# Kernel tuning notes

Hardware: AMD Instinct MI355X
Metric: run time of the kernel (lower is better)

The kernel has to match this reference:

```python
import jax, jax.numpy as jnp
import numpy as np

VOCAB, D_MODEL, DICT, TOP_K = 50257, 512, 16384, 32
N_CONCEPTS, N_RELATIONS = 16, 6
B, S = 1024, 32


def sparse_topk(coeffs, top_k):
    # abs-topk along last dim, keep signed values, scatter to dense
    _, idx = jax.lax.top_k(jnp.abs(coeffs), top_k)          # [B, k]
    signed = jnp.take_along_axis(coeffs, idx, axis=-1)      # [B, k]
    rows = jnp.arange(coeffs.shape[0])[:, None]
    return jnp.zeros_like(coeffs).at[rows, idx].set(signed)


def setup_inputs() -> dict:
    key = jax.random.key(0)
    ks = jax.random.split(key, 16)
    f = lambda k, shape, scale: jax.random.normal(k, shape, dtype=jnp.float32) * scale
    inp = {
        'clean_tokens': jax.random.randint(ks[0], (B, S), 0, VOCAB),
        'noisy_tokens': jax.random.randint(ks[1], (B, S), 0, VOCAB),
        'embedding': f(ks[2], (VOCAB, D_MODEL), 1.0),
        'enc_w1': f(ks[3], (D_MODEL, D_MODEL), D_MODEL ** -0.5),
        'enc_b1': jnp.zeros((D_MODEL,), jnp.float32),
        'enc_w2': f(ks[4], (D_MODEL, D_MODEL), D_MODEL ** -0.5),
        'enc_b2': jnp.zeros((D_MODEL,), jnp.float32),
        'shared_atoms': f(ks[5], (DICT, D_MODEL), 0.04),
        'router_w': f(ks[6], (DICT, D_MODEL), D_MODEL ** -0.5),
        'concept_delta_w': f(ks[7], (DICT, D_MODEL), D_MODEL ** -0.5),
        'relation_delta_w': f(ks[8], (DICT, D_MODEL), D_MODEL ** -0.5),
        'concept_head_w': f(ks[9], (N_CONCEPTS, D_MODEL), D_MODEL ** -0.5),
        'concept_head_b': jnp.zeros((N_CONCEPTS,), jnp.float32),
        'relation_head_w': f(ks[10], (N_RELATIONS, D_MODEL), D_MODEL ** -0.5),
        'relation_head_b': jnp.zeros((N_RELATIONS,), jnp.float32),
    }
    return inp


def reference(clean_tokens, noisy_tokens, embedding, enc_w1, enc_b1, enc_w2, enc_b2,
              shared_atoms, router_w, concept_delta_w, relation_delta_w,
              concept_head_w, concept_head_b, relation_head_w, relation_head_b):
    def pooled(tokens):
        x = embedding[tokens].mean(axis=1)                       # [B, D]
        h = jax.nn.silu(x @ enc_w1.T + enc_b1)
        return h @ enc_w2.T + enc_b2

    def encode(p, delta_w):
        coeffs = p @ router_w.T + 0.3 * (p @ delta_w.T)          # [B, DICT]
        sparse = sparse_topk(coeffs, TOP_K)
        rep = sparse @ shared_atoms                              # [B, D]
        return rep, sparse

    clean_p = pooled(clean_tokens)
    noisy_p = pooled(noisy_tokens)
    c_rep, c_sp = encode(clean_p, concept_delta_w)
    r_rep, r_sp = encode(clean_p, relation_delta_w)
    nc_rep, nc_sp = encode(noisy_p, concept_delta_w)
    nr_rep, nr_sp = encode(noisy_p, relation_delta_w)

    fused_clean = 0.2 * clean_p + 0.9 * c_rep + 0.9 * r_rep
    fused_noisy = 0.2 * noisy_p + 0.9 * nc_rep + 0.9 * nr_rep

    return (fused_clean @ concept_head_w.T + concept_head_b,
            fused_clean @ relation_head_w.T + relation_head_b,
            fused_noisy @ concept_head_w.T + concept_head_b,
            fused_noisy @ relation_head_w.T + relation_head_b,
            c_sp, r_sp, nc_sp, nr_sp)
```

## Files before the change

### kernel.cpp

```cpp
#include <hip/hip_runtime.h>


typedef _Float16 f16x8 __attribute__((ext_vector_type(8)));
typedef _Float16 f16x4 __attribute__((ext_vector_type(4)));
typedef float f32x4 __attribute__((ext_vector_type(4)));

#define OUT_SPARSE 45056
#define SPARSE_PER 16777216

#define ASYNC16(gp, lp) __builtin_amdgcn_global_load_lds(                      \
    (const __attribute__((address_space(1))) void*)(gp),                       \
    (__attribute__((address_space(3))) void*)(lp), 16, 0, 0)

__device__ inline float h2f(unsigned s) {
    _Float16 h = __builtin_bit_cast(_Float16, (unsigned short)(s & 0xFFFFu));
    return (float)h;
}

__global__ __launch_bounds__(128) void pool_kernel(
    const int* __restrict__ ct, const int* __restrict__ nt,
    const float* __restrict__ emb, double* __restrict__ xout)
{
    const int row = blockIdx.x, s = blockIdx.y;
    const int tid = threadIdx.x;
    __shared__ int tk[32];
    const int* t = (s ? nt : ct) + row * 32;
    if (tid < 32) tk[tid] = t[tid];
    __syncthreads();
    const int d = tid * 4;
    double a0 = 0, a1 = 0, a2 = 0, a3 = 0;
    for (int i = 0; i < 32; ++i) {
        const float4 v = *(const float4*)(emb + (size_t)tk[i] * 512 + d);
        a0 += (double)v.x; a1 += (double)v.y; a2 += (double)v.z; a3 += (double)v.w;
    }
    double* o = xout + ((size_t)s * 1024 + row) * 512 + d;
    o[0] = a0 * 0.03125; o[1] = a1 * 0.03125; o[2] = a2 * 0.03125; o[3] = a3 * 0.03125;
}

__global__ __launch_bounds__(256) void enc_gemm(
    const double* __restrict__ A, const float* __restrict__ W,
    const float* __restrict__ bias, double* __restrict__ C,
    _Float16* __restrict__ C16, int act)
{
    __shared__ double Ask[16][68];
    __shared__ double Wsk[16][68];
    const int tid = threadIdx.x;
    const int m0 = blockIdx.y * 64, n0 = blockIdx.x * 64;
    const int ty = tid >> 4, tx = tid & 15;
    const int r = tid >> 2, c4 = (tid & 3) * 4;
    double acc[4][4] = {};
    for (int k0 = 0; k0 < 512; k0 += 16) {
        const double4 av = *(const double4*)(A + (size_t)(m0 + r) * 512 + k0 + c4);
        const float4  wv = *(const float4*) (W + (size_t)(n0 + r) * 512 + k0 + c4);
        __syncthreads();
        Ask[c4 + 0][r] = av.x; Ask[c4 + 1][r] = av.y; Ask[c4 + 2][r] = av.z; Ask[c4 + 3][r] = av.w;
        Wsk[c4 + 0][r] = (double)wv.x; Wsk[c4 + 1][r] = (double)wv.y;
        Wsk[c4 + 2][r] = (double)wv.z; Wsk[c4 + 3][r] = (double)wv.w;
        __syncthreads();
#pragma unroll
        for (int k = 0; k < 16; ++k) {
            const double4 a = *(const double4*)&Ask[k][ty * 4];
            const double4 b = *(const double4*)&Wsk[k][tx * 4];
            const double aa[4] = {a.x, a.y, a.z, a.w};
            const double bb[4] = {b.x, b.y, b.z, b.w};
#pragma unroll
            for (int i = 0; i < 4; ++i)
#pragma unroll
                for (int j = 0; j < 4; ++j) acc[i][j] += aa[i] * bb[j];
        }
    }
#pragma unroll
    for (int i = 0; i < 4; ++i) {
        const int row = m0 + ty * 4 + i;
#pragma unroll
        for (int j = 0; j < 4; ++j) {
            const int col = n0 + tx * 4 + j;
            double v = acc[i][j] + (double)bias[col];
            if (act) v = v / (1.0 + exp(-v));
            C[(size_t)row * 512 + col] = v;
            if (C16) C16[(size_t)row * 512 + col] = (_Float16)v;
        }
    }
}

__global__ __launch_bounds__(256) void combine_kernel(
    const float* __restrict__ router, const float* __restrict__ cd,
    const float* __restrict__ rd, _Float16* __restrict__ wc,
    _Float16* __restrict__ wr, float* __restrict__ wcf,
    float* __restrict__ wrf)
{
    const size_t i = ((size_t)blockIdx.x * 256 + threadIdx.x) * 4;
    if (i >= (size_t)16384 * 512) return;
    const float4 r = *(const float4*)(router + i);
    const float4 c = *(const float4*)(cd + i);
    const float4 d = *(const float4*)(rd + i);
    const float4 fc = { r.x + 0.3f * c.x, r.y + 0.3f * c.y, r.z + 0.3f * c.z, r.w + 0.3f * c.w };
    const float4 fr = { r.x + 0.3f * d.x, r.y + 0.3f * d.y, r.z + 0.3f * d.z, r.w + 0.3f * d.w };
    f16x4 hc = { (_Float16)fc.x, (_Float16)fc.y, (_Float16)fc.z, (_Float16)fc.w };
    f16x4 hr = { (_Float16)fr.x, (_Float16)fr.y, (_Float16)fr.z, (_Float16)fr.w };
    *(f16x4*)(wc + i) = hc;
    *(f16x4*)(wr + i) = hr;
    *(float4*)(wcf + i) = fc;
    *(float4*)(wrf + i) = fr;
}

__global__ __launch_bounds__(256) void approx_gemm(
    const _Float16* __restrict__ P, const _Float16* __restrict__ Wc,
    const _Float16* __restrict__ Wr, unsigned* __restrict__ candg)
{
    __shared__ _Float16 ABs[8192];
    __shared__ _Float16 Cst[128 * 128];
    __shared__ unsigned ecnt[128];
    _Float16* As = ABs;
    _Float16* Bs = ABs + 4096;

    const int tid = threadIdx.x;
    const int q = blockIdx.z;
    const int n0 = blockIdx.x * 128, m0 = blockIdx.y * 128;
    const _Float16* A = P + (size_t)(q >> 1) * 524288;
    const _Float16* B = (q & 1) ? Wr : Wc;

    const int lane = tid & 63, w = tid >> 6;
    const int wm = w & 1, wn = w >> 1;
    const int lr = lane & 15, lk = lane >> 4;

    const int ch0 = w * 2, ch1 = w * 2 + 1;
    const int lrow = lane >> 2, lh = (lane & 3) * 8;
    const _Float16* Ag0 = A + (size_t)(m0 + ch0 * 16 + lrow) * 512 + lh;
    const _Float16* Ag1 = A + (size_t)(m0 + ch1 * 16 + lrow) * 512 + lh;
    const _Float16* Bg0 = B + (size_t)(n0 + ch0 * 16 + lrow) * 512 + lh;
    const _Float16* Bg1 = B + (size_t)(n0 + ch1 * 16 + lrow) * 512 + lh;
    _Float16* Al0 = As + ch0 * 512;
    _Float16* Al1 = As + ch1 * 512;
    _Float16* Bl0 = Bs + ch0 * 512;
    _Float16* Bl1 = Bs + ch1 * 512;

    const f32x4 zero = {0.f, 0.f, 0.f, 0.f};
    f32x4 acc[4][4];
#pragma unroll
    for (int i = 0; i < 4; ++i)
#pragma unroll
        for (int j = 0; j < 4; ++j) acc[i][j] = zero;

    for (int kt = 0; kt < 16; ++kt) {
        const int k0 = kt * 32;
        __syncthreads();
        ASYNC16(Ag0 + k0, Al0);
        ASYNC16(Ag1 + k0, Al1);
        ASYNC16(Bg0 + k0, Bl0);
        ASYNC16(Bg1 + k0, Bl1);
        __syncthreads();
        f16x8 af[4], bf[4];
#pragma unroll
        for (int i = 0; i < 4; ++i) af[i] = *(const f16x8*)(As + (wm * 64 + i * 16 + lr) * 32 + lk * 8);
#pragma unroll
        for (int j = 0; j < 4; ++j) bf[j] = *(const f16x8*)(Bs + (wn * 64 + j * 16 + lr) * 32 + lk * 8);
#pragma unroll
        for (int i = 0; i < 4; ++i)
#pragma unroll
            for (int j = 0; j < 4; ++j)
                acc[i][j] = __builtin_amdgcn_mfma_f32_16x16x32_f16(af[i], bf[j], acc[i][j], 0, 0, 0);
    }
    __syncthreads();
#pragma unroll
    for (int i = 0; i < 4; ++i)
#pragma unroll
        for (int j = 0; j < 4; ++j)
#pragma unroll
            for (int rr = 0; rr < 4; ++rr)
                Cst[(wm * 64 + i * 16 + lk * 4 + rr) * 128 + (wn * 64 + j * 16 + lr)] =
                    (_Float16)acc[i][j][rr];
    if (tid < 128) ecnt[tid] = 0;
    __syncthreads();

    const int r = tid >> 1, h = tid & 1;
    const unsigned* cr = (const unsigned*)(Cst + r * 128 + h * 64);
    float ss = 0.f;
#pragma unroll
    for (int j = 0; j < 32; ++j) {
        const unsigned u = cr[j];
        const float f0 = h2f(u), f1 = h2f(u >> 16);
        ss = fmaf(f0, f0, fmaf(f1, f1, ss));
    }
    ss += __shfl_xor(ss, 1);
    const _Float16 hc = (_Float16)(2.0f * sqrtf(ss * (1.f / 128.f)));
    const unsigned cutk = (unsigned)__builtin_bit_cast(unsigned short, hc) & 0x7FFFu;
    unsigned* emit = (unsigned*)ABs;
    const int colbase = n0 + h * 64;
#pragma unroll
    for (int j = 0; j < 32; ++j) {
        const unsigned u = cr[j];
        const unsigned k0 = u & 0x7FFFu, k1 = (u >> 16) & 0x7FFFu;
        if (k0 >= cutk && k0) {
            const unsigned pos = atomicAdd(&ecnt[r], 1u);
            if (pos < 32u) emit[r * 32 + pos] = (k0 << 16) | (unsigned)(16383 - (colbase + 2 * j));
        }
        if (k1 >= cutk && k1) {
            const unsigned pos = atomicAdd(&ecnt[r], 1u);
            if (pos < 32u) emit[r * 32 + pos] = (k1 << 16) | (unsigned)(16383 - (colbase + 2 * j + 1));
        }
    }
    __syncthreads();
    {
        const unsigned c = min(ecnt[r], 32u);
#pragma unroll
        for (int s2 = 0; s2 < 16; ++s2) {
            const unsigned sl = (unsigned)(h * 16 + s2);
            if (sl >= c) emit[r * 32 + sl] = 0u;
        }
        unsigned* eg = candg + (((size_t)q * 1024 + m0 + r) * 128 + blockIdx.x) * 32;
        const uint4* e4 = (const uint4*)(emit + r * 32 + h * 16);
        uint4* g4 = (uint4*)(eg + h * 16);
        g4[0] = e4[0]; g4[1] = e4[1]; g4[2] = e4[2]; g4[3] = e4[3];
    }
}

__global__ __launch_bounds__(256) void select_kernel(
    const double* __restrict__ pw, const float* __restrict__ wcf,
    const float* __restrict__ wrf, const unsigned* __restrict__ candg,
    const float* __restrict__ atoms, float* __restrict__ selvw,
    int* __restrict__ seliw, float* __restrict__ repw)
{
    constexpr int NCAP = 160, NRE = 64;
    const int row = blockIdx.x, q = blockIdx.y;
    const int pset = q >> 1;
    const int tid = threadIdx.x;

    __shared__ unsigned hist[1024];
    __shared__ unsigned pscan[256];
    __shared__ double prow[512];
    __shared__ unsigned cent[NCAP];
    __shared__ int r64i[NRE];
    __shared__ double cval[NRE];
    __shared__ float selv[32];
    __shared__ int seli[32];
    __shared__ int cnt, bstar;

    const double* prg = pw + ((size_t)pset * 1024 + row) * 512;
    const unsigned* crow = candg + ((size_t)q * 1024 + row) * 4096;

    for (int b = tid; b < 1024; b += 256) hist[b] = 0;
    if (tid == 0) { cnt = 0; bstar = -1; }
    if (tid < NRE) r64i[tid] = 0;
    prow[tid] = prg[tid];
    prow[tid + 256] = prg[tid + 256];

    uint4 cv[4];
#pragma unroll
    for (int p = 0; p < 4; ++p) cv[p] = ((const uint4*)crow)[p * 256 + tid];
    __syncthreads();

#pragma unroll
    for (int p = 0; p < 4; ++p) {
        const unsigned ee[4] = {cv[p].x, cv[p].y, cv[p].z, cv[p].w};
#pragma unroll
        for (int e = 0; e < 4; ++e)
            if (ee[e]) atomicAdd(&hist[ee[e] >> 21], 1u);
    }
    __syncthreads();

    const unsigned h0 = hist[tid * 4], h1 = hist[tid * 4 + 1];
    const unsigned h2 = hist[tid * 4 + 2], h3 = hist[tid * 4 + 3];
    const unsigned l3 = h3, l2 = h2 + l3, l1 = h1 + l2, l0 = h0 + l1;
    pscan[tid] = l0;
    __syncthreads();
    for (int s = 1; s < 256; s <<= 1) {
        const unsigned v = (tid + s < 256) ? pscan[tid + s] : 0u;
        __syncthreads();
        pscan[tid] += v;
        __syncthreads();
    }
    {
        const unsigned above = (tid < 255) ? pscan[tid + 1] : 0u;
        int best = -1;
        if (l0 + above >= 64u) best = tid * 4;
        if (l1 + above >= 64u) best = tid * 4 + 1;
        if (l2 + above >= 64u) best = tid * 4 + 2;
        if (l3 + above >= 64u) best = tid * 4 + 3;
        if (best >= 0) atomicMax(&bstar, best);
    }
    __syncthreads();
    const unsigned kmin = (unsigned)(bstar < 0 ? 1 : bstar) << 5;

#pragma unroll
    for (int p = 0; p < 4; ++p) {
        const unsigned ee[4] = {cv[p].x, cv[p].y, cv[p].z, cv[p].w};
#pragma unroll
        for (int e = 0; e < 4; ++e) {
            if (ee[e] && (ee[e] >> 16) >= kmin) {
                const int pos = atomicAdd(&cnt, 1);
                if (pos < NCAP) cent[pos] = ee[e];
            }
        }
    }
    __syncthreads();
    const int nc = min(cnt, NCAP);

    for (int p = tid; p < nc; p += 256) {
        const unsigned e = cent[p];
        int rr = 0;
        for (int j = 0; j < nc; ++j) rr += (cent[j] > e) ? 1 : 0;
        if (rr < NRE) r64i[rr] = 16383 - (int)(e & 0xFFFFu);
    }
    __syncthreads();

    const float* wsel = (q & 1) ? wrf : wcf;
    const int w = tid >> 6, lane = tid & 63;
    for (int c = w; c < NRE; c += 4) {
        const int idx = r64i[c];
        const float4* rp4 = (const float4*)(wsel + (size_t)idx * 512);
        const float4 r0 = rp4[lane * 2], r1 = rp4[lane * 2 + 1];
        const double* pv = prow + lane * 8;
        double aR = pv[0] * (double)r0.x + pv[1] * (double)r0.y + pv[2] * (double)r0.z + pv[3] * (double)r0.w
                  + pv[4] * (double)r1.x + pv[5] * (double)r1.y + pv[6] * (double)r1.z + pv[7] * (double)r1.w;
        for (int sh = 32; sh > 0; sh >>= 1) aR += __shfl_down(aR, sh);
        if (lane == 0) cval[c] = aR;
    }
    __syncthreads();

    if (tid < NRE) {
        const double av = fabs(cval[tid]);
        const int mi = r64i[tid];
        int rr = 0;
        for (int j = 0; j < NRE; ++j) {
            const double aj = fabs(cval[j]);
            rr += (aj > av || (aj == av && r64i[j] < mi)) ? 1 : 0;
        }
        if (rr < 32) { selv[rr] = (float)cval[tid]; seli[rr] = mi; }
    }
    __syncthreads();
    if (tid < 32) {
        const size_t sb = ((size_t)q * 1024 + row) * 32 + tid;
        selvw[sb] = selv[tid];
        seliw[sb] = seli[tid];
    }

    double a0 = 0, a1 = 0;
    for (int k = 0; k < 32; ++k) {
        const double v = (double)selv[k];
        const float* ar = atoms + (size_t)seli[k] * 512;
        a0 += v * (double)ar[tid];
        a1 += v * (double)ar[tid + 256];
    }
    float* rp = repw + ((size_t)q * 1024 + row) * 512;
    rp[tid] = (float)a0;
    rp[tid + 256] = (float)a1;
}

__global__ __launch_bounds__(256) void zero_kernel(float4* __restrict__ p, unsigned n4)
{
    const float4 z = {0.f, 0.f, 0.f, 0.f};
    unsigned i = blockIdx.x * 256u + threadIdx.x;
    const unsigned stride = gridDim.x * 256u;
    for (; i < n4; i += stride) p[i] = z;
}

__global__ __launch_bounds__(256) void heads_kernel(
    const double* __restrict__ pw, const float* __restrict__ repw,
    const float* __restrict__ chw, const float* __restrict__ chb,
    const float* __restrict__ rhw, const float* __restrict__ rhb,
    const float* __restrict__ selvw, const int* __restrict__ seliw,
    float* __restrict__ out)
{
    const int row = blockIdx.x, s = blockIdx.y;
    const int tid = threadIdx.x;
    __shared__ double fused[512];

    if (tid < 64) {
        const int qq = s * 2 + (tid >> 5), k = tid & 31;
        const size_t sb = ((size_t)qq * 1024 + row) * 32 + k;
        out[(size_t)OUT_SPARSE + (size_t)qq * SPARSE_PER + (size_t)row * 16384 + (size_t)seliw[sb]] = selvw[sb];
    }

    const double* pr = pw + ((size_t)s * 1024 + row) * 512;
    const float* rc = repw + ((size_t)(s * 2 + 0) * 1024 + row) * 512;
    const float* rr = repw + ((size_t)(s * 2 + 1) * 1024 + row) * 512;
    for (int d = tid; d < 512; d += 256)
        fused[d] = 0.2 * pr[d] + 0.9 * (double)rc[d] + 0.9 * (double)rr[d];
    __syncthreads();
    const int w = tid >> 6, lane = tid & 63;
    for (int o = w; o < 22; o += 4) {
        const float* hw2 = (o < 16) ? (chw + (size_t)o * 512) : (rhw + (size_t)(o - 16) * 512);
        double acc = 0;
#pragma unroll
        for (int j = 0; j < 8; ++j) acc += fused[lane + 64 * j] * (double)hw2[lane + 64 * j];
        for (int sh = 32; sh > 0; sh >>= 1) acc += __shfl_down(acc, sh);
        if (lane == 0) {
            if (o < 16) out[(s ? 22528 : 0) + row * 16 + o] = (float)(acc + (double)chb[o]);
            else        out[(s ? 38912 : 16384) + row * 6 + (o - 16)] = (float)(acc + (double)rhb[o - 16]);
        }
    }
}

extern "C" void kernel_launch(void* const* d_in, const int* in_sizes, int n_in,
                              void* d_out, int out_size, void* d_ws, size_t ws_size,
                              hipStream_t stream)
{
    const int*   ctok   = (const int*)d_in[0];
    const int*   ntok   = (const int*)d_in[1];
    const float* emb    = (const float*)d_in[2];
    const float* w1     = (const float*)d_in[3];
    const float* b1     = (const float*)d_in[4];
    const float* w2     = (const float*)d_in[5];
    const float* b2     = (const float*)d_in[6];
    const float* atoms  = (const float*)d_in[7];
    const float* router = (const float*)d_in[8];
    const float* cdelta = (const float*)d_in[9];
    const float* rdelta = (const float*)d_in[10];
    const float* chw    = (const float*)d_in[11];
    const float* chb    = (const float*)d_in[12];
    const float* rhw    = (const float*)d_in[13];
    const float* rhb    = (const float*)d_in[14];
    float* out = (float*)d_out;

    float*    wcf   = out + OUT_SPARSE;
    float*    wrf   = wcf + 8388608;
    unsigned* candg = (unsigned*)(wrf + 8388608);

    double*    xw   = (double*)d_ws;
    double*    hw   = xw + 1048576;
    double*    pw   = hw + 1048576;
    float*     repw = (float*)(pw + 1048576);
    _Float16*  pf16 = (_Float16*)(repw + 2097152);
    _Float16*  wcw  = pf16 + 1048576;
    _Float16*  wrw  = wcw + 8388608;
    float*     selvw = (float*)hw;
    int*       seliw = (int*)(selvw + 131072);

    pool_kernel<<<dim3(1024, 2), 128, 0, stream>>>(ctok, ntok, emb, xw);
    enc_gemm<<<dim3(8, 32), 256, 0, stream>>>(xw, w1, b1, hw, (_Float16*)nullptr, 1);
    enc_gemm<<<dim3(8, 32), 256, 0, stream>>>(hw, w2, b2, pw, pf16, 0);
    combine_kernel<<<8192, 256, 0, stream>>>(router, cdelta, rdelta, wcw, wrw, wcf, wrf);
    approx_gemm<<<dim3(128, 8, 4), 256, 0, stream>>>(pf16, wcw, wrw, candg);
    select_kernel<<<dim3(1024, 4), 256, 0, stream>>>(pw, wcf, wrf, candg, atoms, selvw, seliw, repw);
    zero_kernel<<<2048, 256, 0, stream>>>((float4*)(out + OUT_SPARSE), (unsigned)SPARSE_PER);
    heads_kernel<<<dim3(1024, 2), 256, 0, stream>>>(pw, repw, chw, chb, rhw, rhb, selvw, seliw, out);
}
```

Before: 876.7 us.

## Swizzle 64-wide K tiles, filter candidates in registers, fuse sparse zeroing into heads

Measured after the change: 873.0 us. About the same (-0.4%).

```diff
diff --git a/kernel.cpp b/kernel.cpp
--- a/kernel.cpp
+++ b/kernel.cpp
@@ -11,11 +11,6 @@
 #define ASYNC16(gp, lp) __builtin_amdgcn_global_load_lds(                      \
     (const __attribute__((address_space(1))) void*)(gp),                       \
     (__attribute__((address_space(3))) void*)(lp), 16, 0, 0)
-
-__device__ inline float h2f(unsigned s) {
-    _Float16 h = __builtin_bit_cast(_Float16, (unsigned short)(s & 0xFFFFu));
-    return (float)h;
-}
 
 __global__ __launch_bounds__(128) void pool_kernel(
     const int* __restrict__ ct, const int* __restrict__ nt,
@@ -108,32 +103,38 @@
     const _Float16* __restrict__ P, const _Float16* __restrict__ Wc,
     const _Float16* __restrict__ Wr, unsigned* __restrict__ candg)
 {
-    __shared__ _Float16 ABs[8192];
-    __shared__ _Float16 Cst[128 * 128];
+    __shared__ _Float16 As[8192];
+    __shared__ _Float16 Bs[8192];
+    __shared__ float    ssp[128][2];
+    __shared__ unsigned cutk_s[128];
     __shared__ unsigned ecnt[128];
-    _Float16* As = ABs;
-    _Float16* Bs = ABs + 4096;
 
     const int tid = threadIdx.x;
     const int q = blockIdx.z;
     const int n0 = blockIdx.x * 128, m0 = blockIdx.y * 128;
-    const _Float16* A = P + (size_t)(q >> 1) * 524288;
-    const _Float16* B = (q & 1) ? Wr : Wc;
+    const _Float16* Agbl = P + (size_t)(q >> 1) * 524288;
+    const _Float16* Bgbl = (q & 1) ? Wr : Wc;
 
     const int lane = tid & 63, w = tid >> 6;
     const int wm = w & 1, wn = w >> 1;
     const int lr = lane & 15, lk = lane >> 4;
-
-    const int ch0 = w * 2, ch1 = w * 2 + 1;
-    const int lrow = lane >> 2, lh = (lane & 3) * 8;
-    const _Float16* Ag0 = A + (size_t)(m0 + ch0 * 16 + lrow) * 512 + lh;
-    const _Float16* Ag1 = A + (size_t)(m0 + ch1 * 16 + lrow) * 512 + lh;
-    const _Float16* Bg0 = B + (size_t)(n0 + ch0 * 16 + lrow) * 512 + lh;
-    const _Float16* Bg1 = B + (size_t)(n0 + ch1 * 16 + lrow) * 512 + lh;
-    _Float16* Al0 = As + ch0 * 512;
-    _Float16* Al1 = As + ch1 * 512;
-    _Float16* Bl0 = Bs + ch0 * 512;
-    _Float16* Bl1 = Bs + ch1 * 512;
+    const int xr = lr & 7;
+
+    const int srow = lane >> 3;
+    const int cg = (lane & 7) ^ srow;
+    const _Float16* ag[4];
+    const _Float16* bg[4];
+    _Float16* al[4];
+    _Float16* bl[4];
+#pragma unroll
+    for (int i = 0; i < 4; ++i) {
+        const int G = i * 4 + w;
+        const int rr0 = G * 8 + srow;
+        ag[i] = Agbl + (size_t)(m0 + rr0) * 512 + cg * 8;
+        bg[i] = Bgbl + (size_t)(n0 + rr0) * 512 + cg * 8;
+        al[i] = As + G * 512;
+        bl[i] = Bs + G * 512;
+    }
 
     const f32x4 zero = {0.f, 0.f, 0.f, 0.f};
     f32x4 acc[4][4];
@@ -142,75 +143,82 @@
 #pragma unroll
         for (int j = 0; j < 4; ++j) acc[i][j] = zero;
 
-    for (int kt = 0; kt < 16; ++kt) {
-        const int k0 = kt * 32;
-        __syncthreads();
-        ASYNC16(Ag0 + k0, Al0);
-        ASYNC16(Ag1 + k0, Al1);
-        ASYNC16(Bg0 + k0, Bl0);
-        ASYNC16(Bg1 + k0, Bl1);
-        __syncthreads();
-        f16x8 af[4], bf[4];
-#pragma unroll
-        for (int i = 0; i < 4; ++i) af[i] = *(const f16x8*)(As + (wm * 64 + i * 16 + lr) * 32 + lk * 8);
-#pragma unroll
-        for (int j = 0; j < 4; ++j) bf[j] = *(const f16x8*)(Bs + (wn * 64 + j * 16 + lr) * 32 + lk * 8);
-#pragma unroll
-        for (int i = 0; i < 4; ++i)
+    for (int kt = 0; kt < 8; ++kt) {
+        const int k0 = kt * 64;
+        __syncthreads();
+#pragma unroll
+        for (int i = 0; i < 4; ++i) ASYNC16(ag[i] + k0, al[i]);
+#pragma unroll
+        for (int i = 0; i < 4; ++i) ASYNC16(bg[i] + k0, bl[i]);
+        __syncthreads();
+#pragma unroll
+        for (int kk = 0; kk < 2; ++kk) {
+            f16x8 af[4], bf[4];
+#pragma unroll
+            for (int i = 0; i < 4; ++i)
+                af[i] = *(const f16x8*)(As + (wm * 64 + i * 16 + lr) * 64 + (((kk << 2) | lk) ^ xr) * 8);
 #pragma unroll
             for (int j = 0; j < 4; ++j)
-                acc[i][j] = __builtin_amdgcn_mfma_f32_16x16x32_f16(af[i], bf[j], acc[i][j], 0, 0, 0);
-    }
-    __syncthreads();
+                bf[j] = *(const f16x8*)(Bs + (wn * 64 + j * 16 + lr) * 64 + (((kk << 2) | lk) ^ xr) * 8);
+#pragma unroll
+            for (int i = 0; i < 4; ++i)
+#pragma unroll
+                for (int j = 0; j < 4; ++j)
+                    acc[i][j] = __builtin_amdgcn_mfma_f32_16x16x32_f16(af[i], bf[j], acc[i][j], 0, 0, 0);
+        }
+    }
+
+    if (tid < 128) ecnt[tid] = 0;
 #pragma unroll
     for (int i = 0; i < 4; ++i)
 #pragma unroll
-        for (int j = 0; j < 4; ++j)
-#pragma unroll
-            for (int rr = 0; rr < 4; ++rr)
-                Cst[(wm * 64 + i * 16 + lk * 4 + rr) * 128 + (wn * 64 + j * 16 + lr)] =
-                    (_Float16)acc[i][j][rr];
-    if (tid < 128) ecnt[tid] = 0;
-    __syncthreads();
-
-    const int r = tid >> 1, h = tid & 1;
-    const unsigned* cr = (const unsigned*)(Cst + r * 128 + h * 64);
-    float ss = 0.f;
-#pragma unroll
-    for (int j = 0; j < 32; ++j) {
-        const unsigned u = cr[j];
-        const float f0 = h2f(u), f1 = h2f(u >> 16);
-        ss = fmaf(f0, f0, fmaf(f1, f1, ss));
-    }
-    ss += __shfl_xor(ss, 1);
-    const _Float16 hc = (_Float16)(2.0f * sqrtf(ss * (1.f / 128.f)));
-    const unsigned cutk = (unsigned)__builtin_bit_cast(unsigned short, hc) & 0x7FFFu;
-    unsigned* emit = (unsigned*)ABs;
-    const int colbase = n0 + h * 64;
-#pragma unroll
-    for (int j = 0; j < 32; ++j) {
-        const unsigned u = cr[j];
-        const unsigned k0 = u & 0x7FFFu, k1 = (u >> 16) & 0x7FFFu;
-        if (k0 >= cutk && k0) {
-            const unsigned pos = atomicAdd(&ecnt[r], 1u);
-            if (pos < 32u) emit[r * 32 + pos] = (k0 << 16) | (unsigned)(16383 - (colbase + 2 * j));
-        }
-        if (k1 >= cutk && k1) {
-            const unsigned pos = atomicAdd(&ecnt[r], 1u);
-            if (pos < 32u) emit[r * 32 + pos] = (k1 << 16) | (unsigned)(16383 - (colbase + 2 * j + 1));
-        }
-    }
+        for (int rr = 0; rr < 4; ++rr) {
+            float s = 0.f;
+#pragma unroll
+            for (int j = 0; j < 4; ++j) { const float v = acc[i][j][rr]; s = fmaf(v, v, s); }
+            s += __shfl_xor(s, 1); s += __shfl_xor(s, 2);
+            s += __shfl_xor(s, 4); s += __shfl_xor(s, 8);
+            if (lr == 0) ssp[wm * 64 + i * 16 + lk * 4 + rr][wn] = s;
+        }
+    __syncthreads();
+    if (tid < 128) {
+        const float sig2 = (ssp[tid][0] + ssp[tid][1]) * (1.f / 128.f);
+        const _Float16 hc = (_Float16)(2.0f * sqrtf(sig2));
+        cutk_s[tid] = (unsigned)__builtin_bit_cast(unsigned short, hc) & 0x7FFFu;
+    }
+    __syncthreads();
+
+    unsigned* emit = (unsigned*)As;
+#pragma unroll
+    for (int i = 0; i < 4; ++i)
+#pragma unroll
+        for (int rr = 0; rr < 4; ++rr) {
+            const int row = wm * 64 + i * 16 + lk * 4 + rr;
+            const unsigned ck = cutk_s[row];
+#pragma unroll
+            for (int j = 0; j < 4; ++j) {
+                const float v = acc[i][j][rr];
+                const _Float16 hv = (_Float16)v;
+                const unsigned key = (unsigned)__builtin_bit_cast(unsigned short, hv) & 0x7FFFu;
+                if (key >= ck && key) {
+                    const unsigned pos = atomicAdd(&ecnt[row], 1u);
+                    const int col = n0 + wn * 64 + j * 16 + lr;
+                    if (pos < 32u) emit[row * 32 + pos] = (key << 16) | (unsigned)(16383 - col);
+                }
+            }
+        }
     __syncthreads();
     {
-        const unsigned c = min(ecnt[r], 32u);
+        const int r2 = tid >> 1, h2 = tid & 1;
+        const unsigned c = min(ecnt[r2], 32u);
 #pragma unroll
         for (int s2 = 0; s2 < 16; ++s2) {
-            const unsigned sl = (unsigned)(h * 16 + s2);
-            if (sl >= c) emit[r * 32 + sl] = 0u;
-        }
-        unsigned* eg = candg + (((size_t)q * 1024 + m0 + r) * 128 + blockIdx.x) * 32;
-        const uint4* e4 = (const uint4*)(emit + r * 32 + h * 16);
-        uint4* g4 = (uint4*)(eg + h * 16);
+            const unsigned sl = (unsigned)(h2 * 16 + s2);
+            if (sl >= c) emit[r2 * 32 + sl] = 0u;
+        }
+        unsigned* eg = candg + (((size_t)q * 1024 + m0 + r2) * 128 + blockIdx.x) * 32;
+        const uint4* e4 = (const uint4*)(emit + r2 * 32 + h2 * 16);
+        uint4* g4 = (uint4*)(eg + h2 * 16);
         g4[0] = e4[0]; g4[1] = e4[1]; g4[2] = e4[2]; g4[3] = e4[3];
     }
 }
@@ -347,14 +355,6 @@
     rp[tid + 256] = (float)a1;
 }
 
-__global__ __launch_bounds__(256) void zero_kernel(float4* __restrict__ p, unsigned n4)
-{
-    const float4 z = {0.f, 0.f, 0.f, 0.f};
-    unsigned i = blockIdx.x * 256u + threadIdx.x;
-    const unsigned stride = gridDim.x * 256u;
-    for (; i < n4; i += stride) p[i] = z;
-}
-
 __global__ __launch_bounds__(256) void heads_kernel(
     const double* __restrict__ pw, const float* __restrict__ repw,
     const float* __restrict__ chw, const float* __restrict__ chb,
@@ -366,11 +366,11 @@
     const int tid = threadIdx.x;
     __shared__ double fused[512];
 
-    if (tid < 64) {
-        const int qq = s * 2 + (tid >> 5), k = tid & 31;
-        const size_t sb = ((size_t)qq * 1024 + row) * 32 + k;
-        out[(size_t)OUT_SPARSE + (size_t)qq * SPARSE_PER + (size_t)row * 16384 + (size_t)seliw[sb]] = selvw[sb];
-    }
+    float4* z0 = (float4*)(out + (size_t)OUT_SPARSE + (size_t)(2 * s + 0) * SPARSE_PER + (size_t)row * 16384);
+    float4* z1 = (float4*)(out + (size_t)OUT_SPARSE + (size_t)(2 * s + 1) * SPARSE_PER + (size_t)row * 16384);
+    const float4 z = {0.f, 0.f, 0.f, 0.f};
+#pragma unroll
+    for (int i = 0; i < 16; ++i) { z0[i * 256 + tid] = z; z1[i * 256 + tid] = z; }
 
     const double* pr = pw + ((size_t)s * 1024 + row) * 512;
     const float* rc = repw + ((size_t)(s * 2 + 0) * 1024 + row) * 512;
@@ -378,6 +378,13 @@
     for (int d = tid; d < 512; d += 256)
         fused[d] = 0.2 * pr[d] + 0.9 * (double)rc[d] + 0.9 * (double)rr[d];
     __syncthreads();
+
+    if (tid < 64) {
+        const int qq = s * 2 + (tid >> 5), k = tid & 31;
+        const size_t sb = ((size_t)qq * 1024 + row) * 32 + k;
+        out[(size_t)OUT_SPARSE + (size_t)qq * SPARSE_PER + (size_t)row * 16384 + (size_t)seliw[sb]] = selvw[sb];
+    }
+
     const int w = tid >> 6, lane = tid & 63;
     for (int o = w; o < 22; o += 4) {
         const float* hw2 = (o < 16) ? (chw + (size_t)o * 512) : (rhw + (size_t)(o - 16) * 512);
@@ -433,6 +440,5 @@
     combine_kernel<<<8192, 256, 0, stream>>>(router, cdelta, rdelta, wcw, wrw, wcf, wrf);
     approx_gemm<<<dim3(128, 8, 4), 256, 0, stream>>>(pf16, wcw, wrw, candg);
     select_kernel<<<dim3(1024, 4), 256, 0, stream>>>(pw, wcf, wrf, candg, atoms, selvw, seliw, repw);
-    zero_kernel<<<2048, 256, 0, stream>>>((float4*)(out + OUT_SPARSE), (unsigned)SPARSE_PER);
     heads_kernel<<<dim3(1024, 2), 256, 0, stream>>>(pw, repw, chw, chb, rhw, rhb, selvw, seliw, out);
 }
```
